# Performance work log

Hardware: AMD Instinct MI355X
Metric: run time of the kernel (lower is better)

## Reference

```python
import jax, jax.numpy as jnp
import numpy as np

HIDDEN = 1024
H = 16        # query heads
HK = 4        # kv heads
G = H // HK   # GQA group size
D = 64        # head dim
EPS = 1e-6


def rmsnorm(x, w):
    # normalize over last dim (head_dim)
    var = jnp.mean(jnp.square(x), axis=-1, keepdims=True)
    return x * jax.lax.rsqrt(var + EPS) * w


def setup_inputs() -> dict:
    key = jax.random.key(0)
    ks = jax.random.split(key, 8)
    B, S_KV, S_Q = 2, 4096, 512
    inputs = jax.random.normal(ks[0], (B, S_KV, HIDDEN), dtype=jnp.float32)
    latent = jax.random.normal(ks[1], (B, S_Q, HIDDEN), dtype=jnp.float32)
    # xavier_uniform-style init: limit = sqrt(6/(fan_in+fan_out))
    def xavier(k, shape, gain=1.0):
        fan_out, fan_in = shape
        limit = gain * np.sqrt(6.0 / (fan_in + fan_out))
        return jax.random.uniform(k, shape, jnp.float32, -limit, limit)
    wq = xavier(ks[2], (H * D, HIDDEN))
    wk = xavier(ks[3], (HK * D, HIDDEN))
    wv = xavier(ks[4], (HK * D, HIDDEN))
    wo = xavier(ks[5], (HIDDEN, H * D), gain=1.0 / np.sqrt(2.0))
    q_norm_w = jnp.ones((D,), jnp.float32)
    k_norm_w = jnp.ones((D,), jnp.float32)
    return {"inputs": inputs, "latent": latent, "wq": wq, "wk": wk,
            "wv": wv, "wo": wo, "q_norm_w": q_norm_w, "k_norm_w": k_norm_w}


def reference(inputs, latent, wq, wk, wv, wo, q_norm_w, k_norm_w):
    B, S_q, _ = latent.shape
    S_kv = inputs.shape[1]
    # projections (Linear: x @ W^T)
    q = (latent @ wq.T).reshape(B, S_q, H, D)    # [B,Sq,H,D]
    k = (inputs @ wk.T).reshape(B, S_kv, HK, D)  # [B,Skv,Hk,D]
    v = (inputs @ wv.T).reshape(B, S_kv, HK, D)
    q = rmsnorm(q, q_norm_w)
    k = rmsnorm(k, k_norm_w)
    # GQA without materializing repeated K/V: view q as [B,Hk,G,Sq,D]
    q = q.transpose(0, 2, 1, 3).reshape(B, HK, G, S_q, D)
    k = k.transpose(0, 2, 1, 3)  # [B,Hk,Skv,D]
    v = v.transpose(0, 2, 1, 3)  # [B,Hk,Skv,D]
    # NOTE: no 1/sqrt(D) scaling, faithful to the source module
    scores = jnp.einsum('bkgqd,bksd->bkgqs', q, k)  # [B,Hk,G,Sq,Skv]
    attn = jax.nn.softmax(scores.astype(jnp.float32), axis=-1).astype(q.dtype)
    out = jnp.einsum('bkgqs,bksd->bkgqd', attn, v)  # [B,Hk,G,Sq,D]
    # back to [B,Sq,H*D]
    out = out.reshape(B, H, S_q, D).transpose(0, 2, 1, 3).reshape(B, S_q, H * D)
    return out @ wo.T
```

## Files before the change

kernel.cpp:

```cpp
#include <hip/hip_runtime.h>

#define NB 2
#define SQ 512
#define SKV 4096
#define HID 1024
#define NH 16
#define NHK 4
#define NG 4
#define HD 64
#define EPSF 1e-6f
#define NSPLIT 4
#define RB (NB * NH * SQ)

typedef short v8s __attribute__((ext_vector_type(8)));
typedef short v4s __attribute__((ext_vector_type(4)));
typedef float v4f __attribute__((ext_vector_type(4)));
typedef float v2f __attribute__((ext_vector_type(2)));

static __device__ __forceinline__ short f2bf(float f) {
  unsigned u = __builtin_bit_cast(unsigned, f);
  u += 0x7FFFu + ((u >> 16) & 1u);
  return (short)(u >> 16);
}

static __device__ __forceinline__ v8s lds_frag(const short* lds, int row, int kbyte) {
  return *(const v8s*)((const char*)lds + row * 128 + (kbyte ^ ((row & 7) << 4)));
}

template<int SRC_F32>
static __device__ __forceinline__ void stage_tile(const void* src, int ld,
                                                  int r0, int c0, short* lds, int t) {
#pragma unroll
  for (int i = 0; i < 2; ++i) {
    int flat = t * 8 + i * 2048;
    int row = flat >> 6, col = flat & 63;
    v8s v;
    if (SRC_F32) {
      const float* p = (const float*)src + (size_t)(r0 + row) * ld + c0 + col;
      v4f a = *(const v4f*)p;
      v4f b = *(const v4f*)(p + 4);
      v[0] = f2bf(a[0]); v[1] = f2bf(a[1]); v[2] = f2bf(a[2]); v[3] = f2bf(a[3]);
      v[4] = f2bf(b[0]); v[5] = f2bf(b[1]); v[6] = f2bf(b[2]); v[7] = f2bf(b[3]);
    } else {
      v = *(const v8s*)((const short*)src + (size_t)(r0 + row) * ld + c0 + col);
    }
    *(v8s*)((char*)lds + row * 128 + ((col * 2) ^ ((row & 7) << 4))) = v;
  }
}

template<int KIND>
__global__ __launch_bounds__(256) void proj_kernel(const float* __restrict__ A,
                                                   const float* __restrict__ W,
                                                   const float* __restrict__ wn,
                                                   short* __restrict__ out) {
  const int S = (KIND == 0) ? SQ : SKV;
  const int LB = (KIND == 0) ? 9 : 12;
  const int nh = (KIND == 0) ? NH : NHK;
  __shared__ __align__(16) short Asm[64 * 64];
  __shared__ __align__(16) short Bsm[64 * 64];
  const int t = threadIdx.x, lane = t & 63, w = t >> 6;
  const int l15 = lane & 15, g4 = lane >> 4;
  const int m0 = blockIdx.x * 64;
  const int h = blockIdx.y;
  v4f acc[4] = {};
  for (int k0 = 0; k0 < HID; k0 += 64) {
    __syncthreads();
    stage_tile<1>(A, HID, m0, k0, Asm, t);
    stage_tile<1>(W, HID, h * 64, k0, Bsm, t);
    __syncthreads();
    const short* asrc = (KIND == 2) ? Bsm : Asm;
    const short* bsrc = (KIND == 2) ? Asm : Bsm;
    v8s af[2];
#pragma unroll
    for (int s = 0; s < 2; ++s)
      af[s] = lds_frag(asrc, w * 16 + l15, s * 64 + g4 * 16);
#pragma unroll
    for (int nf = 0; nf < 4; ++nf)
#pragma unroll
      for (int s = 0; s < 2; ++s) {
        v8s bf = lds_frag(bsrc, nf * 16 + l15, s * 64 + g4 * 16);
        acc[nf] = __builtin_amdgcn_mfma_f32_16x16x32_bf16(af[s], bf, acc[nf], 0, 0, 0);
      }
  }
  if (KIND != 2) {
    float wcol[4];
#pragma unroll
    for (int nf = 0; nf < 4; ++nf) wcol[nf] = wn[nf * 16 + l15];
#pragma unroll
    for (int r = 0; r < 4; ++r) {
      float ss = acc[0][r] * acc[0][r] + acc[1][r] * acc[1][r] +
                 acc[2][r] * acc[2][r] + acc[3][r] * acc[3][r];
#pragma unroll
      for (int msk = 1; msk < 16; msk <<= 1) ss += __shfl_xor(ss, msk);
      float sc = rsqrtf(ss * (1.0f / 64.0f) + EPSF);
      int m = m0 + w * 16 + g4 * 4 + r;
      int b = m >> LB, sl = m & (S - 1);
      size_t base = ((size_t)(b * nh + h) * S + sl) * 64;
#pragma unroll
      for (int nf = 0; nf < 4; ++nf)
        out[base + nf * 16 + l15] = f2bf(acc[nf][r] * sc * wcol[nf]);
    }
  } else {
#pragma unroll
    for (int r = 0; r < 4; ++r) {
      int d = w * 16 + g4 * 4 + r;
#pragma unroll
      for (int nf = 0; nf < 4; ++nf) {
        int skv = m0 + nf * 16 + l15;
        int b = skv >> 12, sl = skv & (SKV - 1);
        out[((size_t)(b * NHK + h) * 64 + d) * SKV + sl] = f2bf(acc[nf][r]);
      }
    }
  }
}

__global__ __launch_bounds__(256) void gemm_bt(const short* __restrict__ Ap,
                                               const float* __restrict__ Bp,
                                               float* __restrict__ C,
                                               int M, int N, int K) {
  __shared__ __align__(16) short Asm[64 * 64];
  __shared__ __align__(16) short Bsm[64 * 64];
  const int t = threadIdx.x;
  const int lane = t & 63, w = t >> 6;
  const int l15 = lane & 15, g4 = lane >> 4;
  const int m0 = blockIdx.x * 64, n0 = blockIdx.y * 64;
  const int wr = (w >> 1) * 32, wc = (w & 1) * 32;
  v4f acc[2][2] = {};
  for (int k0 = 0; k0 < K; k0 += 64) {
    __syncthreads();
    stage_tile<0>(Ap, K, m0, k0, Asm, t);
    stage_tile<1>(Bp, K, n0, k0, Bsm, t);
    __syncthreads();
    v8s af[2][2], bfr[2][2];
#pragma unroll
    for (int mf = 0; mf < 2; ++mf)
#pragma unroll
      for (int s = 0; s < 2; ++s)
        af[mf][s] = lds_frag(Asm, wr + mf * 16 + l15, s * 64 + g4 * 16);
#pragma unroll
    for (int nf = 0; nf < 2; ++nf)
#pragma unroll
      for (int s = 0; s < 2; ++s)
        bfr[nf][s] = lds_frag(Bsm, wc + nf * 16 + l15, s * 64 + g4 * 16);
#pragma unroll
    for (int mf = 0; mf < 2; ++mf)
#pragma unroll
      for (int nf = 0; nf < 2; ++nf)
#pragma unroll
        for (int s = 0; s < 2; ++s)
          acc[mf][nf] = __builtin_amdgcn_mfma_f32_16x16x32_bf16(af[mf][s], bfr[nf][s],
                                                                acc[mf][nf], 0, 0, 0);
  }
#pragma unroll
  for (int mf = 0; mf < 2; ++mf)
#pragma unroll
    for (int nf = 0; nf < 2; ++nf)
#pragma unroll
      for (int r = 0; r < 4; ++r) {
        int row = wr + mf * 16 + g4 * 4 + r;
        int col = wc + nf * 16 + l15;
        C[(size_t)(m0 + row) * N + n0 + col] = acc[mf][nf][r];
      }
}

__global__ __launch_bounds__(256) void attn_kernel(const short* __restrict__ Qb,
                                                   const short* __restrict__ Kb,
                                                   const short* __restrict__ Vt,
                                                   float* __restrict__ Op,
                                                   float* __restrict__ Ml) {
  __shared__ __align__(16) short Ksm[2][64 * 64];
  __shared__ __align__(16) short Vsm[2][64 * 64];
  __shared__ __align__(16) short Psm[4][16 * 64];
  int id = blockIdx.x;
  int qt = id & 31, hk = (id >> 5) & 3, b = (id >> 7) & 1, sp = id >> 8;
  int t = threadIdx.x, w = t >> 6, lane = t & 63;
  int l15 = lane & 15, g4 = lane >> 4;
  int h = hk * NG + w;

  const short* qbase = Qb + (((size_t)(b * NH + h)) * SQ + qt * 16) * 64;
  v8s aq[2];
#pragma unroll
  for (int s = 0; s < 2; ++s)
    aq[s] = *(const v8s*)(qbase + (size_t)l15 * 64 + s * 32 + g4 * 8);

  const short* kbase = Kb + ((size_t)(b * NHK + hk)) * SKV * 64;
  const short* vbase = Vt + ((size_t)(b * NHK + hk)) * 64 * SKV;
  char* pbase = (char*)&Psm[w][0];

  v4f acco[4] = {};
  float mrow[4], lrow[4];
#pragma unroll
  for (int r = 0; r < 4; ++r) { mrow[r] = -__builtin_inff(); lrow[r] = 0.f; }

  const int KV0 = sp * (SKV / NSPLIT);
  for (int kt = 0; kt < SKV / NSPLIT / 128; ++kt) {
    int kv0 = KV0 + kt * 128;
    __syncthreads();
    stage_tile<0>(kbase, 64, kv0, 0, Ksm[0], t);
    stage_tile<0>(kbase, 64, kv0 + 64, 0, Ksm[1], t);
    stage_tile<0>(vbase, SKV, 0, kv0, Vsm[0], t);
    stage_tile<0>(vbase, SKV, 0, kv0 + 64, Vsm[1], t);
    __syncthreads();

    v4f accs[8] = {};
#pragma unroll
    for (int hf = 0; hf < 2; ++hf)
#pragma unroll
      for (int f = 0; f < 4; ++f)
#pragma unroll
        for (int s = 0; s < 2; ++s) {
          v8s bk = lds_frag(Ksm[hf], f * 16 + l15, s * 64 + g4 * 16);
          accs[hf * 4 + f] =
              __builtin_amdgcn_mfma_f32_16x16x32_bf16(aq[s], bk, accs[hf * 4 + f], 0, 0, 0);
        }

    float tm[4];
#pragma unroll
    for (int r = 0; r < 4; ++r) {
      float m01 = fmaxf(accs[0][r], accs[1][r]), m23 = fmaxf(accs[2][r], accs[3][r]);
      float m45 = fmaxf(accs[4][r], accs[5][r]), m67 = fmaxf(accs[6][r], accs[7][r]);
      tm[r] = fmaxf(fmaxf(m01, m23), fmaxf(m45, m67));
    }
#pragma unroll
    for (int msk = 1; msk < 16; msk <<= 1)
#pragma unroll
      for (int r = 0; r < 4; ++r)
        tm[r] = fmaxf(tm[r], __shfl_xor(tm[r], msk));
    float al[4];
#pragma unroll
    for (int r = 0; r < 4; ++r) {
      float mn = fmaxf(mrow[r], tm[r]);
      al[r] = __expf(mrow[r] - mn);
      mrow[r] = mn;
    }
    float rs[4] = {0.f, 0.f, 0.f, 0.f};
#pragma unroll
    for (int f = 0; f < 8; ++f)
#pragma unroll
      for (int r = 0; r < 4; ++r) {
        accs[f][r] = __expf(accs[f][r] - mrow[r]);
        rs[r] += accs[f][r];
      }
#pragma unroll
    for (int msk = 1; msk < 16; msk <<= 1)
#pragma unroll
      for (int r = 0; r < 4; ++r) rs[r] += __shfl_xor(rs[r], msk);
#pragma unroll
    for (int r = 0; r < 4; ++r) lrow[r] = lrow[r] * al[r] + rs[r];
#pragma unroll
    for (int fd = 0; fd < 4; ++fd)
#pragma unroll
      for (int r = 0; r < 4; ++r) acco[fd][r] *= al[r];

#pragma unroll
    for (int hf = 0; hf < 2; ++hf) {
#pragma unroll
      for (int f = 0; f < 4; ++f)
#pragma unroll
        for (int r = 0; r < 4; ++r) {
          int row = g4 * 4 + r;
          int colB = (f * 16 + l15) * 2;
          *(short*)(pbase + row * 128 + (colB ^ ((row & 7) << 4))) = f2bf(accs[hf * 4 + f][r]);
        }
      asm volatile("s_waitcnt lgkmcnt(0)" ::: "memory");
      __builtin_amdgcn_sched_barrier(0);
      v8s pa[2];
#pragma unroll
      for (int s = 0; s < 2; ++s)
        pa[s] = *(const v8s*)(pbase + l15 * 128 + ((s * 64 + g4 * 16) ^ ((l15 & 7) << 4)));
      asm volatile("s_waitcnt lgkmcnt(0)" ::: "memory");
      __builtin_amdgcn_sched_barrier(0);
#pragma unroll
      for (int fd = 0; fd < 4; ++fd)
#pragma unroll
        for (int s = 0; s < 2; ++s) {
          v8s vb = lds_frag(Vsm[hf], fd * 16 + l15, s * 64 + g4 * 16);
          acco[fd] = __builtin_amdgcn_mfma_f32_16x16x32_bf16(pa[s], vb, acco[fd], 0, 0, 0);
        }
    }
  }

  size_t rowbase = ((size_t)b * NH + h) * SQ + qt * 16;
#pragma unroll
  for (int fd = 0; fd < 4; ++fd)
#pragma unroll
    for (int r = 0; r < 4; ++r) {
      int row = g4 * 4 + r;
      Op[((size_t)sp * RB + rowbase + row) * 64 + fd * 16 + l15] = acco[fd][r];
    }
  if (l15 == 0) {
#pragma unroll
    for (int r = 0; r < 4; ++r) {
      int row = g4 * 4 + r;
      v2f ml; ml[0] = mrow[r]; ml[1] = lrow[r];
      *(v2f*)(Ml + ((size_t)sp * RB + rowbase + row) * 2) = ml;
    }
  }
}

__global__ __launch_bounds__(256) void merge_attn(const float* __restrict__ Op,
                                                  const float* __restrict__ Ml,
                                                  short* __restrict__ Ab) {
  int idx = blockIdx.x * 256 + threadIdx.x;
  int d = idx & 63, row = idx >> 6;
  float ms[NSPLIT], ls[NSPLIT];
  float M = -__builtin_inff();
#pragma unroll
  for (int s = 0; s < NSPLIT; ++s) {
    v2f ml = *(const v2f*)(Ml + ((size_t)s * RB + row) * 2);
    ms[s] = ml[0]; ls[s] = ml[1];
    M = fmaxf(M, ms[s]);
  }
  float L = 0.f, o = 0.f;
#pragma unroll
  for (int s = 0; s < NSPLIT; ++s) {
    float wgt = __expf(ms[s] - M);
    L += ls[s] * wgt;
    o += wgt * Op[((size_t)s * RB + row) * 64 + d];
  }
  int b = row >> 13;
  int hh = (row >> 9) & 15;
  int sq = row & 511;
  Ab[((size_t)(b * SQ + sq)) * HID + hh * 64 + d] = f2bf(o / L);
}

extern "C" void kernel_launch(void* const* d_in, const int* in_sizes, int n_in,
                              void* d_out, int out_size, void* d_ws, size_t ws_size,
                              hipStream_t stream) {
  const float* inputs = (const float*)d_in[0];
  const float* latent = (const float*)d_in[1];
  const float* wq = (const float*)d_in[2];
  const float* wk = (const float*)d_in[3];
  const float* wv = (const float*)d_in[4];
  const float* wo = (const float*)d_in[5];
  const float* qnw = (const float*)d_in[6];
  const float* knw = (const float*)d_in[7];

  char* ws = (char*)d_ws;
  float* Op  = (float*)(ws);
  float* Ml  = (float*)(ws + 16777216);
  short* Qb  = (short*)(ws + 17825792);
  short* Kb  = (short*)(ws + 19922944);
  short* Vtb = (short*)(ws + 24117248);
  short* Ab  = (short*)(ws + 28311552);

  proj_kernel<0><<<dim3(16, 16), 256, 0, stream>>>(latent, wq, qnw, Qb);
  proj_kernel<1><<<dim3(128, 4), 256, 0, stream>>>(inputs, wk, knw, Kb);
  proj_kernel<2><<<dim3(128, 4), 256, 0, stream>>>(inputs, wv, knw, Vtb);
  attn_kernel<<<256 * NSPLIT, 256, 0, stream>>>(Qb, Kb, Vtb, Op, Ml);
  merge_attn<<<RB * 64 / 256, 256, 0, stream>>>(Op, Ml, Ab);
  gemm_bt<<<dim3(16, 16), 256, 0, stream>>>(Ab, wo, (float*)d_out, 1024, 1024, 1024);
}
```

Measured before the change: 247.3 us.

## Enlarge projection GEMM tiles and merge K/V projections into one launch

Replaces the per-head 64x64 projection kernels with larger tiles: K and V projections share one 128x128-tile kernel launched over a z dimension, and the Q and output projections use a 64x128 tile kernel. The V-transpose store is vectorised to 4-element writes. The aim is more reuse of each staged fp32 input tile per MFMA and fewer launches. In exchange the grids are smaller (256 blocks for K/V, 128 for Q/out), which may underfill the GPU, and register pressure rises.

After: 240.8 us. 1.03x faster.

```diff
diff --git a/kernel.cpp b/kernel.cpp
--- a/kernel.cpp
+++ b/kernel.cpp
@@ -27,11 +27,11 @@
   return *(const v8s*)((const char*)lds + row * 128 + (kbyte ^ ((row & 7) << 4)));
 }
 
-template<int SRC_F32>
+template<int SRC_F32, int NIT>
 static __device__ __forceinline__ void stage_tile(const void* src, int ld,
                                                   int r0, int c0, short* lds, int t) {
 #pragma unroll
-  for (int i = 0; i < 2; ++i) {
+  for (int i = 0; i < NIT; ++i) {
     int flat = t * 8 + i * 2048;
     int row = flat >> 6, col = flat & 63;
     v8s v;
@@ -48,119 +48,155 @@
   }
 }
 
-template<int KIND>
-__global__ __launch_bounds__(256) void proj_kernel(const float* __restrict__ A,
-                                                   const float* __restrict__ W,
-                                                   const float* __restrict__ wn,
-                                                   short* __restrict__ out) {
-  const int S = (KIND == 0) ? SQ : SKV;
-  const int LB = (KIND == 0) ? 9 : 12;
-  const int nh = (KIND == 0) ? NH : NHK;
-  __shared__ __align__(16) short Asm[64 * 64];
-  __shared__ __align__(16) short Bsm[64 * 64];
+__global__ __launch_bounds__(256) void proj_kv(const float* __restrict__ A,
+                                               const float* __restrict__ Wk,
+                                               const float* __restrict__ Wv,
+                                               const float* __restrict__ knw,
+                                               short* __restrict__ Kb,
+                                               short* __restrict__ Vtb) {
+  __shared__ __align__(16) short Asm[128 * 64];
+  __shared__ __align__(16) short Bsm[128 * 64];
   const int t = threadIdx.x, lane = t & 63, w = t >> 6;
   const int l15 = lane & 15, g4 = lane >> 4;
-  const int m0 = blockIdx.x * 64;
-  const int h = blockIdx.y;
-  v4f acc[4] = {};
+  const int wr = w >> 1, wc = w & 1;
+  const int m0 = blockIdx.x * 128, n0 = blockIdx.y * 128;
+  const int isV = blockIdx.z;
+  const float* W = isV ? Wv : Wk;
+  v4f acc[4][4] = {};
   for (int k0 = 0; k0 < HID; k0 += 64) {
     __syncthreads();
-    stage_tile<1>(A, HID, m0, k0, Asm, t);
-    stage_tile<1>(W, HID, h * 64, k0, Bsm, t);
-    __syncthreads();
-    const short* asrc = (KIND == 2) ? Bsm : Asm;
-    const short* bsrc = (KIND == 2) ? Asm : Bsm;
-    v8s af[2];
-#pragma unroll
-    for (int s = 0; s < 2; ++s)
-      af[s] = lds_frag(asrc, w * 16 + l15, s * 64 + g4 * 16);
+    stage_tile<1, 4>(A, HID, m0, k0, Asm, t);
+    stage_tile<1, 4>(W, HID, n0, k0, Bsm, t);
+    __syncthreads();
+    v8s af[4][2], bfr[4][2];
+#pragma unroll
+    for (int mf = 0; mf < 4; ++mf)
+#pragma unroll
+      for (int s = 0; s < 2; ++s)
+        af[mf][s] = lds_frag(Asm, wr * 64 + mf * 16 + l15, s * 64 + g4 * 16);
 #pragma unroll
     for (int nf = 0; nf < 4; ++nf)
 #pragma unroll
-      for (int s = 0; s < 2; ++s) {
-        v8s bf = lds_frag(bsrc, nf * 16 + l15, s * 64 + g4 * 16);
-        acc[nf] = __builtin_amdgcn_mfma_f32_16x16x32_bf16(af[s], bf, acc[nf], 0, 0, 0);
-      }
-  }
-  if (KIND != 2) {
-    float wcol[4];
-#pragma unroll
-    for (int nf = 0; nf < 4; ++nf) wcol[nf] = wn[nf * 16 + l15];
-#pragma unroll
-    for (int r = 0; r < 4; ++r) {
-      float ss = acc[0][r] * acc[0][r] + acc[1][r] * acc[1][r] +
-                 acc[2][r] * acc[2][r] + acc[3][r] * acc[3][r];
-#pragma unroll
-      for (int msk = 1; msk < 16; msk <<= 1) ss += __shfl_xor(ss, msk);
-      float sc = rsqrtf(ss * (1.0f / 64.0f) + EPSF);
-      int m = m0 + w * 16 + g4 * 4 + r;
-      int b = m >> LB, sl = m & (S - 1);
-      size_t base = ((size_t)(b * nh + h) * S + sl) * 64;
+      for (int s = 0; s < 2; ++s)
+        bfr[nf][s] = lds_frag(Bsm, wc * 64 + nf * 16 + l15, s * 64 + g4 * 16);
+#pragma unroll
+    for (int mf = 0; mf < 4; ++mf)
 #pragma unroll
       for (int nf = 0; nf < 4; ++nf)
-        out[base + nf * 16 + l15] = f2bf(acc[nf][r] * sc * wcol[nf]);
-    }
-  } else {
-#pragma unroll
-    for (int r = 0; r < 4; ++r) {
-      int d = w * 16 + g4 * 4 + r;
-#pragma unroll
-      for (int nf = 0; nf < 4; ++nf) {
-        int skv = m0 + nf * 16 + l15;
-        int b = skv >> 12, sl = skv & (SKV - 1);
-        out[((size_t)(b * NHK + h) * 64 + d) * SKV + sl] = f2bf(acc[nf][r]);
-      }
-    }
-  }
-}
-
-__global__ __launch_bounds__(256) void gemm_bt(const short* __restrict__ Ap,
-                                               const float* __restrict__ Bp,
-                                               float* __restrict__ C,
-                                               int M, int N, int K) {
-  __shared__ __align__(16) short Asm[64 * 64];
-  __shared__ __align__(16) short Bsm[64 * 64];
-  const int t = threadIdx.x;
-  const int lane = t & 63, w = t >> 6;
-  const int l15 = lane & 15, g4 = lane >> 4;
-  const int m0 = blockIdx.x * 64, n0 = blockIdx.y * 64;
-  const int wr = (w >> 1) * 32, wc = (w & 1) * 32;
-  v4f acc[2][2] = {};
-  for (int k0 = 0; k0 < K; k0 += 64) {
-    __syncthreads();
-    stage_tile<0>(Ap, K, m0, k0, Asm, t);
-    stage_tile<1>(Bp, K, n0, k0, Bsm, t);
-    __syncthreads();
-    v8s af[2][2], bfr[2][2];
-#pragma unroll
-    for (int mf = 0; mf < 2; ++mf)
-#pragma unroll
-      for (int s = 0; s < 2; ++s)
-        af[mf][s] = lds_frag(Asm, wr + mf * 16 + l15, s * 64 + g4 * 16);
-#pragma unroll
-    for (int nf = 0; nf < 2; ++nf)
-#pragma unroll
-      for (int s = 0; s < 2; ++s)
-        bfr[nf][s] = lds_frag(Bsm, wc + nf * 16 + l15, s * 64 + g4 * 16);
-#pragma unroll
-    for (int mf = 0; mf < 2; ++mf)
-#pragma unroll
-      for (int nf = 0; nf < 2; ++nf)
 #pragma unroll
         for (int s = 0; s < 2; ++s)
           acc[mf][nf] = __builtin_amdgcn_mfma_f32_16x16x32_bf16(af[mf][s], bfr[nf][s],
                                                                 acc[mf][nf], 0, 0, 0);
   }
-#pragma unroll
-  for (int mf = 0; mf < 2; ++mf)
-#pragma unroll
-    for (int nf = 0; nf < 2; ++nf)
-#pragma unroll
-      for (int r = 0; r < 4; ++r) {
-        int row = wr + mf * 16 + g4 * 4 + r;
-        int col = wc + nf * 16 + l15;
-        C[(size_t)(m0 + row) * N + n0 + col] = acc[mf][nf][r];
-      }
+  const int head = blockIdx.y * 2 + wc;
+  if (!isV) {
+    float wcol[4];
+#pragma unroll
+    for (int nf = 0; nf < 4; ++nf) wcol[nf] = knw[nf * 16 + l15];
+#pragma unroll
+    for (int mf = 0; mf < 4; ++mf)
+#pragma unroll
+      for (int j = 0; j < 4; ++j) {
+        float ss = acc[mf][0][j] * acc[mf][0][j] + acc[mf][1][j] * acc[mf][1][j] +
+                   acc[mf][2][j] * acc[mf][2][j] + acc[mf][3][j] * acc[mf][3][j];
+#pragma unroll
+        for (int msk = 1; msk < 16; msk <<= 1) ss += __shfl_xor(ss, msk);
+        float sc = rsqrtf(ss * (1.0f / 64.0f) + EPSF);
+        int m = m0 + wr * 64 + mf * 16 + g4 * 4 + j;
+        int b = m >> 12, sl = m & (SKV - 1);
+        size_t base = ((size_t)(b * NHK + head) * SKV + sl) * 64;
+#pragma unroll
+        for (int nf = 0; nf < 4; ++nf)
+          Kb[base + nf * 16 + l15] = f2bf(acc[mf][nf][j] * sc * wcol[nf]);
+      }
+  } else {
+#pragma unroll
+    for (int mf = 0; mf < 4; ++mf) {
+      int m = m0 + wr * 64 + mf * 16 + g4 * 4;
+      int b = m >> 12, sl = m & (SKV - 1);
+#pragma unroll
+      for (int nf = 0; nf < 4; ++nf) {
+        int d = nf * 16 + l15;
+        v4s o;
+#pragma unroll
+        for (int j = 0; j < 4; ++j) o[j] = f2bf(acc[mf][nf][j]);
+        *(v4s*)(Vtb + ((size_t)(b * NHK + head) * 64 + d) * SKV + sl) = o;
+      }
+    }
+  }
+}
+
+template<int KIND>
+__global__ __launch_bounds__(256) void gemm64(const void* __restrict__ Ap,
+                                              const float* __restrict__ W,
+                                              const float* __restrict__ wn,
+                                              void* __restrict__ outp) {
+  __shared__ __align__(16) short Asm[64 * 64];
+  __shared__ __align__(16) short Bsm[128 * 64];
+  const int t = threadIdx.x, lane = t & 63, w = t >> 6;
+  const int l15 = lane & 15, g4 = lane >> 4;
+  const int wr = w >> 1, wc = w & 1;
+  const int m0 = blockIdx.x * 64, n0 = blockIdx.y * 128;
+  v4f acc[2][4] = {};
+  for (int k0 = 0; k0 < HID; k0 += 64) {
+    __syncthreads();
+    stage_tile<(KIND == 0) ? 1 : 0, 2>(Ap, HID, m0, k0, Asm, t);
+    stage_tile<1, 4>(W, HID, n0, k0, Bsm, t);
+    __syncthreads();
+    v8s af[2][2], bfr[4][2];
+#pragma unroll
+    for (int mf = 0; mf < 2; ++mf)
+#pragma unroll
+      for (int s = 0; s < 2; ++s)
+        af[mf][s] = lds_frag(Asm, wr * 32 + mf * 16 + l15, s * 64 + g4 * 16);
+#pragma unroll
+    for (int nf = 0; nf < 4; ++nf)
+#pragma unroll
+      for (int s = 0; s < 2; ++s)
+        bfr[nf][s] = lds_frag(Bsm, wc * 64 + nf * 16 + l15, s * 64 + g4 * 16);
+#pragma unroll
+    for (int mf = 0; mf < 2; ++mf)
+#pragma unroll
+      for (int nf = 0; nf < 4; ++nf)
+#pragma unroll
+        for (int s = 0; s < 2; ++s)
+          acc[mf][nf] = __builtin_amdgcn_mfma_f32_16x16x32_bf16(af[mf][s], bfr[nf][s],
+                                                                acc[mf][nf], 0, 0, 0);
+  }
+  if (KIND == 0) {
+    short* outb = (short*)outp;
+    const int head = blockIdx.y * 2 + wc;
+    float wcol[4];
+#pragma unroll
+    for (int nf = 0; nf < 4; ++nf) wcol[nf] = wn[nf * 16 + l15];
+#pragma unroll
+    for (int mf = 0; mf < 2; ++mf)
+#pragma unroll
+      for (int j = 0; j < 4; ++j) {
+        float ss = acc[mf][0][j] * acc[mf][0][j] + acc[mf][1][j] * acc[mf][1][j] +
+                   acc[mf][2][j] * acc[mf][2][j] + acc[mf][3][j] * acc[mf][3][j];
+#pragma unroll
+        for (int msk = 1; msk < 16; msk <<= 1) ss += __shfl_xor(ss, msk);
+        float sc = rsqrtf(ss * (1.0f / 64.0f) + EPSF);
+        int m = m0 + wr * 32 + mf * 16 + g4 * 4 + j;
+        int b = m >> 9, sl = m & (SQ - 1);
+        size_t base = ((size_t)(b * NH + head) * SQ + sl) * 64;
+#pragma unroll
+        for (int nf = 0; nf < 4; ++nf)
+          outb[base + nf * 16 + l15] = f2bf(acc[mf][nf][j] * sc * wcol[nf]);
+      }
+  } else {
+    float* C = (float*)outp;
+#pragma unroll
+    for (int mf = 0; mf < 2; ++mf)
+#pragma unroll
+      for (int j = 0; j < 4; ++j) {
+        int m = m0 + wr * 32 + mf * 16 + g4 * 4 + j;
+#pragma unroll
+        for (int nf = 0; nf < 4; ++nf)
+          C[(size_t)m * HID + n0 + wc * 64 + nf * 16 + l15] = acc[mf][nf][j];
+      }
+  }
 }
 
 __global__ __launch_bounds__(256) void attn_kernel(const short* __restrict__ Qb,
@@ -196,10 +232,10 @@
   for (int kt = 0; kt < SKV / NSPLIT / 128; ++kt) {
     int kv0 = KV0 + kt * 128;
     __syncthreads();
-    stage_tile<0>(kbase, 64, kv0, 0, Ksm[0], t);
-    stage_tile<0>(kbase, 64, kv0 + 64, 0, Ksm[1], t);
-    stage_tile<0>(vbase, SKV, 0, kv0, Vsm[0], t);
-    stage_tile<0>(vbase, SKV, 0, kv0 + 64, Vsm[1], t);
+    stage_tile<0, 2>(kbase, 64, kv0, 0, Ksm[0], t);
+    stage_tile<0, 2>(kbase, 64, kv0 + 64, 0, Ksm[1], t);
+    stage_tile<0, 2>(vbase, SKV, 0, kv0, Vsm[0], t);
+    stage_tile<0, 2>(vbase, SKV, 0, kv0 + 64, Vsm[1], t);
     __syncthreads();
 
     v4f accs[8] = {};
@@ -344,10 +380,9 @@
   short* Vtb = (short*)(ws + 24117248);
   short* Ab  = (short*)(ws + 28311552);
 
-  proj_kernel<0><<<dim3(16, 16), 256, 0, stream>>>(latent, wq, qnw, Qb);
-  proj_kernel<1><<<dim3(128, 4), 256, 0, stream>>>(inputs, wk, knw, Kb);
-  proj_kernel<2><<<dim3(128, 4), 256, 0, stream>>>(inputs, wv, knw, Vtb);
+  gemm64<0><<<dim3(16, 8), 256, 0, stream>>>(latent, wq, qnw, Qb);
+  proj_kv<<<dim3(64, 2, 2), 256, 0, stream>>>(inputs, wk, wv, knw, Kb, Vtb);
   attn_kernel<<<256 * NSPLIT, 256, 0, stream>>>(Qb, Kb, Vtb, Op, Ml);
   merge_attn<<<RB * 64 / 256, 256, 0, stream>>>(Op, Ml, Ab);
-  gemm_bt<<<dim3(16, 16), 256, 0, stream>>>(Ab, wo, (float*)d_out, 1024, 1024, 1024);
-}
+  gemm64<1><<<dim3(16, 8), 256, 0, stream>>>(Ab, wo, nullptr, (float*)d_out);
+}
```
